# Optimization experiments

Measured on AMD Instinct MI355X. Metric: run time of the kernel, lower is better.

Reference implementation:

```python
import jax, jax.numpy as jnp
import numpy as np

B, T, C, HS = 8, 4096, 512, 64

def setup_inputs() -> dict:
    key = jax.random.key(0)
    k1, k2, k3, k4 = jax.random.split(key, 4)
    x = jax.random.normal(k1, (B, T, C), dtype=jnp.float32)
    # causal mask (lower-triangular), int32: 1 = keep, 0 = mask out
    mask = jnp.tril(jnp.ones((T, T), dtype=jnp.int32))
    Wk = jax.random.normal(k2, (C, HS), dtype=jnp.float32) * (1.0 / np.sqrt(C))
    Wq = jax.random.normal(k3, (C, HS), dtype=jnp.float32) * (1.0 / np.sqrt(C))
    Wv = jax.random.normal(k4, (C, HS), dtype=jnp.float32) * (1.0 / np.sqrt(C))
    return {"x": x, "mask": mask, "Wk": Wk, "Wq": Wq, "Wv": Wv}

def reference(x, mask, Wk, Wq, Wv):
    # single self-attention head; scale uses C (n_embd), matching the source
    k = jnp.einsum('btc,ch->bth', x, Wk)   # [B,T,HS]
    q = jnp.einsum('btc,ch->bth', x, Wq)
    v = jnp.einsum('btc,ch->bth', x, Wv)
    scale = x.shape[-1] ** -0.5
    wei = jnp.einsum('bth,bsh->bts', q, k) * scale          # [B,T,T]
    wei = jnp.where(mask == 0, jnp.float32(-1e9), wei)
    wei = jax.nn.softmax(wei, axis=-1)
    # dropout is identity in eval mode
    out = jnp.einsum('bts,bsh->bth', wei, v)                # [B,T,HS]
    return out
```

## Files before the change

kernel.cpp:

```cpp
#include <hip/hip_runtime.h>
#include <hip/hip_bf16.h>
#include <stdint.h>

typedef unsigned short u16;
typedef __bf16 bf16x8_t __attribute__((ext_vector_type(8)));
typedef __bf16 bf16x4_t __attribute__((ext_vector_type(4)));
typedef float f32x4_t __attribute__((ext_vector_type(4)));
typedef float f32x8_t __attribute__((ext_vector_type(8)));

#define TSEQ 4096
#define CDIM 512
#define HSD  64
#define NBATCH 8

static __device__ __forceinline__ f32x4_t mfma16(bf16x8_t a, bf16x8_t b, f32x4_t c) {
  return __builtin_amdgcn_mfma_f32_16x16x32_bf16(a, b, c, 0, 0, 0);
}

static __device__ __forceinline__ u16 f2bf(float f) {
  union { __bf16 h; u16 s; } v; v.h = (__bf16)f;
  return v.s;
}
static __device__ __forceinline__ float bf2f(u16 h) {
  union { unsigned u; float f; } v; v.u = ((unsigned)h) << 16;
  return v.f;
}
static __device__ __forceinline__ bf16x8_t pack8(const float* p) {
  f32x8_t v = *(const f32x8_t*)p;
  return __builtin_convertvector(v, bf16x8_t);
}
static __device__ __forceinline__ bf16x4_t cvt4(f32x4_t v) {
  return __builtin_convertvector(v, bf16x4_t);
}

static __device__ __forceinline__ void gload16(const void* g, void* l) {
  __builtin_amdgcn_global_load_lds(
      (const __attribute__((address_space(1))) unsigned int*)g,
      (__attribute__((address_space(3))) unsigned int*)l, 16, 0, 0);
}

#define QSCALE (0.044194173824159216f * 1.4426950408889634f)
#define MFIX 32.0f

__global__ __launch_bounds__(256) void repack_w(const float* __restrict__ Wk,
                                                const float* __restrict__ Wq,
                                                const float* __restrict__ Wv,
                                                u16* __restrict__ pw) {
  int i = blockIdx.x * 256 + threadIdx.x;
  int j    = i & 7;
  int l15  = (i >> 3) & 15;
  int quad = (i >> 7) & 3;
  int f    = i >> 9;
  int kc   = f / 12;
  int n12  = f - kc * 12;
  int m    = n12 >> 2;
  int n    = n12 & 3;
  const float* W = (m == 0) ? Wk : ((m == 1) ? Wq : Wv);
  pw[i] = f2bf(W[(kc * 32 + quad * 8 + j) * HSD + n * 16 + l15]);
}

__global__ __launch_bounds__(256, 2) void proj_kernel(const float* __restrict__ x,
                                                      const u16* __restrict__ pw,
                                                      u16* __restrict__ kb,
                                                      u16* __restrict__ qb,
                                                      u16* __restrict__ vb,
                                                      u16* __restrict__ vbT,
                                                      int split) {
  const int tid = threadIdx.x;
  const int lane = tid & 63;
  const int wave = tid >> 6;
  const int l15 = lane & 15, quad = lane >> 4;
  const int rblk = (int)blockIdx.x;
  const int rowLocal = wave * 16 + l15;

  __shared__ __align__(16) char SMEM[61440];
  float (*XS)[2048] = (float (*)[2048])SMEM;
  u16   (*PS)[6144] = (u16 (*)[6144])(SMEM + 24576);
  u16* VtS = (u16*)SMEM;

  const float* xg = x + (size_t)rblk * 64 * CDIM;

  const int xrow = tid >> 3;
  const int xch  = tid & 7;

  f32x4_t acc[12];
#pragma unroll
  for (int n = 0; n < 12; ++n) acc[n] = f32x4_t{0.f, 0.f, 0.f, 0.f};

  auto STAGE = [&](int slot, int kc) {
#pragma unroll
    for (int p = 0; p < 2; ++p) {
      const float* src = xg + (size_t)(p * 32 + xrow) * CDIM + kc * 32 + xch * 4;
      gload16(src, (char*)&XS[slot][0] + p * 4096 + tid * 16);
    }
#pragma unroll
    for (int r = 0; r < 3; ++r) {
      int f = r * 256 + tid;
      gload16(pw + (size_t)kc * 6144 + (size_t)f * 8, (char*)&PS[slot][0] + f * 16);
    }
  };

  STAGE(0, 0);
  STAGE(1, 1);

  int slot = 0;
  for (int kc = 0; kc < 16; ++kc) {
    if (kc < 15) asm volatile("s_waitcnt vmcnt(5)" ::: "memory");
    else         asm volatile("s_waitcnt vmcnt(0)" ::: "memory");
    __builtin_amdgcn_s_barrier();

    if (kc + 2 < 16) {
      int s2 = slot + 2; if (s2 >= 3) s2 -= 3;
      STAGE(s2, kc + 2);
    }

    f32x8_t xv = *(const f32x8_t*)&XS[slot][rowLocal * 32 + quad * 8];
    bf16x8_t a = __builtin_convertvector(xv, bf16x8_t);
#pragma unroll
    for (int n12 = 0; n12 < 12; ++n12) {
      bf16x8_t b = *(const bf16x8_t*)&PS[slot][((n12 * 4 + quad) * 16 + l15) * 8];
      acc[n12] = mfma16(a, b, acc[n12]);
    }

    ++slot; if (slot >= 3) slot = 0;
  }

  const int row_base = rblk * 64 + wave * 16 + quad * 4;
#pragma unroll
  for (int n = 0; n < 4; ++n) {
#pragma unroll
    for (int r = 0; r < 4; ++r) {
      kb[(size_t)(row_base + r) * HSD + n * 16 + l15] = f2bf(acc[n][r]);
      qb[(size_t)(row_base + r) * HSD + n * 16 + l15] = f2bf(acc[4 + n][r] * QSCALE);
    }
  }

  if (!split) {
#pragma unroll
    for (int n = 0; n < 4; ++n)
#pragma unroll
      for (int r = 0; r < 4; ++r)
        vb[(size_t)(row_base + r) * HSD + n * 16 + l15] = f2bf(acc[8 + n][r]);
  } else {
    __syncthreads();
#pragma unroll
    for (int n = 0; n < 4; ++n) {
      int h = n * 16 + l15;
      int tl = wave * 16 + quad * 4;
      *(bf16x4_t*)&VtS[h * 72 + tl] = cvt4(acc[8 + n]);
    }
    __syncthreads();
    const int bb = (rblk * 64) >> 12;
    const int t0 = (rblk * 64) & 4095;
#pragma unroll
    for (int it = 0; it < 2; ++it) {
      int g = it * 256 + tid;
      int h = g >> 3;
      int cc = g & 7;
      bf16x8_t vv = *(const bf16x8_t*)&VtS[h * 72 + cc * 8];
      *(bf16x8_t*)&vbT[(size_t)(bb * HSD + h) * TSEQ + t0 + cc * 8] = vv;
    }
  }
}

__global__ __launch_bounds__(256, 3) void attn_part(const u16* __restrict__ qb,
                                                    const u16* __restrict__ kb,
                                                    const u16* __restrict__ vbT,
                                                    u16* __restrict__ pO,
                                                    float* __restrict__ pl) {
  const int e = 287 - (int)blockIdx.x;
  int g = 0;
  while (g < 7 && 4 * (g + 1) * (g + 2) <= e) ++g;
  int local = e - 4 * g * (g + 1);
  int qtl = 0;
  while (local >= g + 1) { local -= g + 1; ++qtl; }
  const int qt = 8 * g + qtl;
  const int c  = local;

  const int b = blockIdx.y;
  const int tid = threadIdx.x;
  const int lane = tid & 63;
  const int wave = tid >> 6;
  const int l15 = lane & 15, quad = lane >> 4;

  __shared__ __align__(16) u16 Ks[128 * 72];
  __shared__ __align__(16) u16 Vt[64 * 136];
  __shared__ __align__(16) u16 Ps[4][16 * 72];

  const size_t bo = (size_t)b * TSEQ * HSD;
  const u16* qp = qb + bo;
  const u16* kp = kb + bo;
  const u16* vtp = vbT + (size_t)b * HSD * TSEQ;

  const int qglob = qt * 64 + wave * 16 + l15;
  bf16x8_t qf0 = *(const bf16x8_t*)(qp + (size_t)qglob * HSD + quad * 8);
  bf16x8_t qf1 = *(const bf16x8_t*)(qp + (size_t)qglob * HSD + 32 + quad * 8);

  f32x4_t o[4];
#pragma unroll
  for (int n = 0; n < 4; ++n) o[n] = f32x4_t{0.f, 0.f, 0.f, 0.f};
  float lsum = 0.f;

  const int st_lo = c * 8;
  const int nt = min(qt - st_lo + 1, 8);
  const int npair = (nt + 1) >> 1;

  const int kr = tid >> 3;
  const int kc8 = (tid & 7) * 8;
  const int vr = tid >> 4;
  const int vc8 = (tid & 15) * 8;

  u16* myP = Ps[wave];

  const f32x4_t sinit = f32x4_t{-MFIX, -MFIX, -MFIX, -MFIX};

  bf16x8_t kst[4], vst[4];
  {
    const int s64 = st_lo * 64;
#pragma unroll
    for (int p = 0; p < 4; ++p) {
      kst[p] = *(const bf16x8_t*)(kp + (size_t)(s64 + kr + 32 * p) * HSD + kc8);
      vst[p] = *(const bf16x8_t*)(vtp + (size_t)(vr + 16 * p) * TSEQ + s64 + vc8);
    }
  }

  for (int ip = 0; ip < npair; ++ip) {
    __syncthreads();
#pragma unroll
    for (int p = 0; p < 4; ++p) {
      *(bf16x8_t*)&Ks[(kr + 32 * p) * 72 + kc8] = kst[p];
      *(bf16x8_t*)&Vt[(vr + 16 * p) * 136 + vc8] = vst[p];
    }
    if (ip + 1 < npair) {
      const int s64 = (st_lo + 2 * (ip + 1)) * 64;
#pragma unroll
      for (int p = 0; p < 4; ++p) {
        kst[p] = *(const bf16x8_t*)(kp + (size_t)(s64 + kr + 32 * p) * HSD + kc8);
        vst[p] = *(const bf16x8_t*)(vtp + (size_t)(vr + 16 * p) * TSEQ + s64 + vc8);
      }
    }
    __syncthreads();

    const int st0 = st_lo + 2 * ip;
    const int nsub = (2 * ip + 1 < nt) ? 2 : 1;
#pragma unroll 2
    for (int hs = 0; hs < nsub; ++hs) {
      const int stx = st0 + hs;
      const int roff = hs * 64;

      f32x4_t s[4];
#pragma unroll
      for (int n = 0; n < 4; ++n) {
        bf16x8_t a0 = *(const bf16x8_t*)&Ks[(roff + n * 16 + l15) * 72 + quad * 8];
        bf16x8_t a1 = *(const bf16x8_t*)&Ks[(roff + n * 16 + l15) * 72 + 32 + quad * 8];
        f32x4_t a = sinit;
        a = mfma16(a0, qf0, a);
        a = mfma16(a1, qf1, a);
        s[n] = a;
      }

      if (stx == qt) {
#pragma unroll
        for (int n = 0; n < 4; ++n) {
          int sg = stx * 64 + n * 16 + quad * 4;
#pragma unroll
          for (int r = 0; r < 4; ++r)
            if (sg + r > qglob) s[n][r] = -1e9f;
        }
      }

#pragma unroll
      for (int n = 0; n < 4; ++n) {
        f32x4_t pv;
        pv[0] = exp2f(s[n][0]);
        pv[1] = exp2f(s[n][1]);
        pv[2] = exp2f(s[n][2]);
        pv[3] = exp2f(s[n][3]);
        lsum += (pv[0] + pv[1]) + (pv[2] + pv[3]);
        *(bf16x4_t*)&myP[l15 * 72 + n * 16 + quad * 4] = cvt4(pv);
      }

      asm volatile("s_waitcnt lgkmcnt(0)" ::: "memory");

#pragma unroll
      for (int kc = 0; kc < 2; ++kc) {
        bf16x8_t pf = *(const bf16x8_t*)&myP[l15 * 72 + kc * 32 + quad * 8];
#pragma unroll
        for (int n = 0; n < 4; ++n) {
          bf16x8_t vf = *(const bf16x8_t*)&Vt[(n * 16 + l15) * 136 + roff + kc * 32 + quad * 8];
          o[n] = mfma16(pf, vf, o[n]);
        }
      }
    }
  }

  lsum += __shfl_xor(lsum, 16);
  lsum += __shfl_xor(lsum, 32);

  const int pidx = (b * 64 + qt) * 8 + c;
  u16* po = pO + (size_t)pidx * 4096;
  float* pm = pl + (size_t)pidx * 64;
#pragma unroll
  for (int n = 0; n < 4; ++n)
#pragma unroll
    for (int r = 0; r < 4; ++r)
      po[(wave * 16 + quad * 4 + r) * 64 + n * 16 + l15] = f2bf(o[n][r]);
  if (lane < 16) pm[wave * 16 + lane] = lsum;
}

__global__ __launch_bounds__(256) void attn_combine(const u16* __restrict__ pO,
                                                    const float* __restrict__ pl,
                                                    float* __restrict__ out) {
  const int tid = threadIdx.x;
  const int h2 = tid & 31;
  const int rr = tid >> 5;
  const int rowg = blockIdx.x * 8 + rr;
  const int b = rowg >> 12;
  const int t = rowg & 4095;
  const int qt = t >> 6;
  const int tr = t & 63;
  const int nc = (qt >> 3) + 1;
  const int pbase = (b * 64 + qt) * 8;

  const unsigned* pO32 = (const unsigned*)pO;
  float o0 = 0.f, o1 = 0.f, lsum = 0.f;
  for (int cc = 0; cc < nc; ++cc) {
    lsum += pl[(size_t)(pbase + cc) * 64 + tr];
    unsigned u = pO32[(size_t)(pbase + cc) * 2048 + tr * 32 + h2];
    o0 += bf2f((u16)(u & 0xffffu));
    o1 += bf2f((u16)(u >> 16));
  }
  float2 res;
  res.x = o0 / lsum;
  res.y = o1 / lsum;
  *(float2*)&out[(size_t)rowg * HSD + h2 * 2] = res;
}

__global__ __launch_bounds__(256) void attn_single(const u16* __restrict__ qb,
                                                   const u16* __restrict__ kb,
                                                   const u16* __restrict__ vb,
                                                   float* __restrict__ out) {
  const int qt = (int)gridDim.x - 1 - (int)blockIdx.x;
  const int b = blockIdx.y;
  const int lane = threadIdx.x & 63;
  const int wave = threadIdx.x >> 6;
  const int l15 = lane & 15, quad = lane >> 4;

  __shared__ __align__(16) u16 Ks[64 * 72];
  __shared__ __align__(16) u16 Vt[64 * 72];
  __shared__ __align__(16) u16 Ps[4][16 * 72];

  const size_t bo = (size_t)b * TSEQ * HSD;
  const u16* qp = qb + bo;
  const u16* kp = kb + bo;
  const u16* vp = vb + bo;

  const int qrow0 = qt * 64 + wave * 16;
  bf16x8_t qf0 = *(const bf16x8_t*)(qp + (size_t)(qrow0 + l15) * HSD + quad * 8);
  bf16x8_t qf1 = *(const bf16x8_t*)(qp + (size_t)(qrow0 + l15) * HSD + 32 + quad * 8);

  f32x4_t o[4];
#pragma unroll
  for (int n = 0; n < 4; ++n) o[n] = f32x4_t{0.f, 0.f, 0.f, 0.f};
  float lrow[4] = {0.f, 0.f, 0.f, 0.f};

  const int ldr = threadIdx.x >> 3;
  const int ldc = (threadIdx.x & 7) * 8;

  const f32x4_t sinit = f32x4_t{-MFIX, -MFIX, -MFIX, -MFIX};

  for (int st = 0; st <= qt; ++st) {
    const int s0 = st * 64;
#pragma unroll
    for (int pp = 0; pp < 2; ++pp) {
      int r = ldr + pp * 32;
      bf16x8_t kv = *(const bf16x8_t*)(kp + (size_t)(s0 + r) * HSD + ldc);
      *(bf16x8_t*)&Ks[r * 72 + ldc] = kv;
      bf16x8_t vv = *(const bf16x8_t*)(vp + (size_t)(s0 + r) * HSD + ldc);
      const u16* vu = (const u16*)&vv;
#pragma unroll
      for (int j = 0; j < 8; ++j) Vt[(ldc + j) * 72 + r] = vu[j];
    }
    __syncthreads();

    f32x4_t s[4];
#pragma unroll
    for (int n = 0; n < 4; ++n) {
      bf16x8_t k0 = *(const bf16x8_t*)&Ks[(n * 16 + l15) * 72 + quad * 8];
      bf16x8_t k1 = *(const bf16x8_t*)&Ks[(n * 16 + l15) * 72 + 32 + quad * 8];
      f32x4_t a = sinit;
      a = mfma16(qf0, k0, a);
      a = mfma16(qf1, k1, a);
      s[n] = a;
    }

    if (st == qt) {
#pragma unroll
      for (int n = 0; n < 4; ++n) {
        int sg = s0 + n * 16 + l15;
#pragma unroll
        for (int r = 0; r < 4; ++r) {
          int tg = qrow0 + quad * 4 + r;
          if (sg > tg) s[n][r] = -1e9f;
        }
      }
    }

#pragma unroll
    for (int n = 0; n < 4; ++n)
#pragma unroll
      for (int r = 0; r < 4; ++r) {
        float p = exp2f(s[n][r]);
        s[n][r] = p;
        lrow[r] += p;
      }

    u16* myP = Ps[wave];
#pragma unroll
    for (int n = 0; n < 4; ++n)
#pragma unroll
      for (int r = 0; r < 4; ++r)
        myP[(quad * 4 + r) * 72 + n * 16 + l15] = f2bf(s[n][r]);

    __syncthreads();

#pragma unroll
    for (int kc = 0; kc < 2; ++kc) {
      bf16x8_t pf = *(const bf16x8_t*)&myP[l15 * 72 + kc * 32 + quad * 8];
#pragma unroll
      for (int n = 0; n < 4; ++n) {
        bf16x8_t vf = *(const bf16x8_t*)&Vt[(n * 16 + l15) * 72 + kc * 32 + quad * 8];
        o[n] = mfma16(pf, vf, o[n]);
      }
    }
    __syncthreads();
  }

#pragma unroll
  for (int r = 0; r < 4; ++r) {
    float l = lrow[r];
    l += __shfl_xor(l, 1);
    l += __shfl_xor(l, 2);
    l += __shfl_xor(l, 4);
    l += __shfl_xor(l, 8);
    lrow[r] = l;
  }

#pragma unroll
  for (int n = 0; n < 4; ++n)
#pragma unroll
    for (int r = 0; r < 4; ++r)
      out[bo + (size_t)(qrow0 + quad * 4 + r) * HSD + n * 16 + l15] = o[n][r] / lrow[r];
}

extern "C" void kernel_launch(void* const* d_in, const int* in_sizes, int n_in,
                              void* d_out, int out_size, void* d_ws, size_t ws_size,
                              hipStream_t stream) {
  const float* x  = (const float*)d_in[0];
  const float* Wk = (const float*)d_in[2];
  const float* Wq = (const float*)d_in[3];
  const float* Wv = (const float*)d_in[4];
  float* out = (float*)d_out;

  char* base = (char*)d_ws;
  const size_t KV = (size_t)NBATCH * TSEQ * HSD;
  u16* pw  = (u16*)base;
  u16* kb  = (u16*)(base + (1 << 18));
  u16* qb  = kb + KV;
  u16* vbT = qb + KV;
  u16* pO  = vbT + KV;
  u16* vb  = pO;
  float* pl = (float*)(pO + (size_t)4096 * 4096);
  const size_t need = (size_t)(1 << 18) + 3 * KV * 2
                    + (size_t)4096 * 4096 * 2
                    + (size_t)4096 * 64 * 4;
  const int split = (ws_size >= need) ? 1 : 0;

  hipLaunchKernelGGL(repack_w, dim3(384), dim3(256), 0, stream, Wk, Wq, Wv, pw);
  hipLaunchKernelGGL(proj_kernel, dim3(512), dim3(256), 0, stream, x, pw, kb, qb, vb, vbT, split);
  if (split) {
    hipLaunchKernelGGL(attn_part, dim3(288, NBATCH), dim3(256), 0, stream, qb, kb, vbT, pO, pl);
    hipLaunchKernelGGL(attn_combine, dim3(4096), dim3(256), 0, stream, pO, pl, out);
  } else {
    hipLaunchKernelGGL(attn_single, dim3(64, NBATCH), dim3(256), 0, stream, qb, kb, vb, out);
  }
}
```

Baseline: 195.9 us.

## Use 32x32 MFMA with 128-row query tiles and permlane P transfer

The attention-part kernel moves from 16x16x32 MFMA on 64-query tiles to 32x32x16 MFMA on 128-query tiles, so each block shares one K/V staging pass across twice as many queries and the grid is halved. The P matrix no longer round-trips through shared memory: it is rearranged in registers with permlane32_swap to form the A operand of the PV MFMA, which removes the Ps buffer and its LDS waits. Per-wave diagonal skipping drops key tiles that lie beyond a wave's causal limit. Occupancy is raised to 4 blocks per SM. The trade-offs are more accumulator registers and possibly coarser load balance across blocks.

```diff
diff --git a/kernel.cpp b/kernel.cpp
--- a/kernel.cpp
+++ b/kernel.cpp
@@ -7,6 +7,8 @@
 typedef __bf16 bf16x4_t __attribute__((ext_vector_type(4)));
 typedef float f32x4_t __attribute__((ext_vector_type(4)));
 typedef float f32x8_t __attribute__((ext_vector_type(8)));
+typedef float f32x16_t __attribute__((ext_vector_type(16)));
+typedef int i32x2_t __attribute__((ext_vector_type(2)));
 
 #define TSEQ 4096
 #define CDIM 512
@@ -15,6 +17,9 @@
 
 static __device__ __forceinline__ f32x4_t mfma16(bf16x8_t a, bf16x8_t b, f32x4_t c) {
   return __builtin_amdgcn_mfma_f32_16x16x32_bf16(a, b, c, 0, 0, 0);
+}
+static __device__ __forceinline__ f32x16_t mfma32(bf16x8_t a, bf16x8_t b, f32x16_t c) {
+  return __builtin_amdgcn_mfma_f32_32x32x16_bf16(a, b, c, 0, 0, 0);
 }
 
 static __device__ __forceinline__ u16 f2bf(float f) {
@@ -163,56 +168,56 @@
   }
 }
 
-__global__ __launch_bounds__(256, 3) void attn_part(const u16* __restrict__ qb,
+__global__ __launch_bounds__(256, 4) void attn_part(const u16* __restrict__ qb,
                                                     const u16* __restrict__ kb,
                                                     const u16* __restrict__ vbT,
                                                     u16* __restrict__ pO,
                                                     float* __restrict__ pl) {
-  const int e = 287 - (int)blockIdx.x;
+  const int e = 143 - (int)blockIdx.x;
   int g = 0;
-  while (g < 7 && 4 * (g + 1) * (g + 2) <= e) ++g;
-  int local = e - 4 * g * (g + 1);
+  while (g < 7 && 2 * (g + 1) * (g + 2) <= e) ++g;
+  int local = e - 2 * g * (g + 1);
   int qtl = 0;
   while (local >= g + 1) { local -= g + 1; ++qtl; }
-  const int qt = 8 * g + qtl;
-  const int c  = local;
+  const int qt2 = 4 * g + qtl;
+  const int c   = local;
 
   const int b = blockIdx.y;
   const int tid = threadIdx.x;
   const int lane = tid & 63;
   const int wave = tid >> 6;
-  const int l15 = lane & 15, quad = lane >> 4;
+  const int l31 = lane & 31;
+  const int h2  = lane >> 5;
 
   __shared__ __align__(16) u16 Ks[128 * 72];
   __shared__ __align__(16) u16 Vt[64 * 136];
-  __shared__ __align__(16) u16 Ps[4][16 * 72];
 
   const size_t bo = (size_t)b * TSEQ * HSD;
   const u16* qp = qb + bo;
   const u16* kp = kb + bo;
   const u16* vtp = vbT + (size_t)b * HSD * TSEQ;
 
-  const int qglob = qt * 64 + wave * 16 + l15;
-  bf16x8_t qf0 = *(const bf16x8_t*)(qp + (size_t)qglob * HSD + quad * 8);
-  bf16x8_t qf1 = *(const bf16x8_t*)(qp + (size_t)qglob * HSD + 32 + quad * 8);
-
-  f32x4_t o[4];
-#pragma unroll
-  for (int n = 0; n < 4; ++n) o[n] = f32x4_t{0.f, 0.f, 0.f, 0.f};
+  const int qglob = qt2 * 128 + wave * 32 + l31;
+  const int wdiag = (qt2 * 128 + wave * 32 + 31) >> 6;
+
+  bf16x8_t qf[4];
+#pragma unroll
+  for (int kk = 0; kk < 4; ++kk)
+    qf[kk] = *(const bf16x8_t*)(qp + (size_t)qglob * HSD + kk * 16 + h2 * 8);
+
+  f32x16_t o0, o1;
+#pragma unroll
+  for (int i = 0; i < 16; ++i) { o0[i] = 0.f; o1[i] = 0.f; }
   float lsum = 0.f;
 
   const int st_lo = c * 8;
-  const int nt = min(qt - st_lo + 1, 8);
+  const int nt = min(2 * qt2 + 2 - st_lo, 8);
   const int npair = (nt + 1) >> 1;
 
   const int kr = tid >> 3;
   const int kc8 = (tid & 7) * 8;
   const int vr = tid >> 4;
   const int vc8 = (tid & 15) * 8;
-
-  u16* myP = Ps[wave];
-
-  const f32x4_t sinit = f32x4_t{-MFIX, -MFIX, -MFIX, -MFIX};
 
   bf16x8_t kst[4], vst[4];
   {
@@ -246,66 +251,71 @@
 #pragma unroll 2
     for (int hs = 0; hs < nsub; ++hs) {
       const int stx = st0 + hs;
+      if (stx > wdiag) continue;
       const int roff = hs * 64;
 
-      f32x4_t s[4];
-#pragma unroll
-      for (int n = 0; n < 4; ++n) {
-        bf16x8_t a0 = *(const bf16x8_t*)&Ks[(roff + n * 16 + l15) * 72 + quad * 8];
-        bf16x8_t a1 = *(const bf16x8_t*)&Ks[(roff + n * 16 + l15) * 72 + 32 + quad * 8];
-        f32x4_t a = sinit;
-        a = mfma16(a0, qf0, a);
-        a = mfma16(a1, qf1, a);
-        s[n] = a;
-      }
-
-      if (stx == qt) {
-#pragma unroll
-        for (int n = 0; n < 4; ++n) {
-          int sg = stx * 64 + n * 16 + quad * 4;
-#pragma unroll
-          for (int r = 0; r < 4; ++r)
-            if (sg + r > qglob) s[n][r] = -1e9f;
+#pragma unroll
+      for (int st2 = 0; st2 < 2; ++st2) {
+        f32x16_t s;
+#pragma unroll
+        for (int i = 0; i < 16; ++i) s[i] = -MFIX;
+#pragma unroll
+        for (int kk = 0; kk < 4; ++kk) {
+          bf16x8_t a = *(const bf16x8_t*)&Ks[(roff + st2 * 32 + l31) * 72 + kk * 16 + h2 * 8];
+          s = mfma32(a, qf[kk], s);
+        }
+
+        if (stx == wdiag) {
+#pragma unroll
+          for (int i = 0; i < 16; ++i) {
+            int sg = stx * 64 + st2 * 32 + 4 * h2 + (i & 3) + 8 * (i >> 2);
+            if (sg > qglob) s[i] = -1e9f;
+          }
+        }
+
+#pragma unroll
+        for (int i = 0; i < 16; ++i) s[i] = exp2f(s[i]);
+#pragma unroll
+        for (int i = 0; i < 16; i += 4)
+          lsum += ((s[i] + s[i + 1]) + (s[i + 2] + s[i + 3]));
+
+        union { bf16x4_t v; int d[2]; } X[4];
+#pragma unroll
+        for (int m = 0; m < 4; ++m) {
+          f32x4_t t;
+          t[0] = s[4 * m]; t[1] = s[4 * m + 1]; t[2] = s[4 * m + 2]; t[3] = s[4 * m + 3];
+          X[m].v = cvt4(t);
+        }
+
+#pragma unroll
+        for (int kkl = 0; kkl < 2; ++kkl) {
+          i32x2_t r0 = __builtin_amdgcn_permlane32_swap(X[2 * kkl].d[0], X[2 * kkl + 1].d[0], false, false);
+          i32x2_t r1 = __builtin_amdgcn_permlane32_swap(X[2 * kkl].d[1], X[2 * kkl + 1].d[1], false, false);
+          union { bf16x8_t v; int d[4]; } af;
+          af.d[0] = r0[0]; af.d[1] = r1[0];
+          af.d[2] = r0[1]; af.d[3] = r1[1];
+          const int kkg = st2 * 2 + kkl;
+          bf16x8_t vf0 = *(const bf16x8_t*)&Vt[l31 * 136 + roff + kkg * 16 + h2 * 8];
+          bf16x8_t vf1 = *(const bf16x8_t*)&Vt[(32 + l31) * 136 + roff + kkg * 16 + h2 * 8];
+          o0 = mfma32(af.v, vf0, o0);
+          o1 = mfma32(af.v, vf1, o1);
         }
       }
-
-#pragma unroll
-      for (int n = 0; n < 4; ++n) {
-        f32x4_t pv;
-        pv[0] = exp2f(s[n][0]);
-        pv[1] = exp2f(s[n][1]);
-        pv[2] = exp2f(s[n][2]);
-        pv[3] = exp2f(s[n][3]);
-        lsum += (pv[0] + pv[1]) + (pv[2] + pv[3]);
-        *(bf16x4_t*)&myP[l15 * 72 + n * 16 + quad * 4] = cvt4(pv);
-      }
-
-      asm volatile("s_waitcnt lgkmcnt(0)" ::: "memory");
-
-#pragma unroll
-      for (int kc = 0; kc < 2; ++kc) {
-        bf16x8_t pf = *(const bf16x8_t*)&myP[l15 * 72 + kc * 32 + quad * 8];
-#pragma unroll
-        for (int n = 0; n < 4; ++n) {
-          bf16x8_t vf = *(const bf16x8_t*)&Vt[(n * 16 + l15) * 136 + roff + kc * 32 + quad * 8];
-          o[n] = mfma16(pf, vf, o[n]);
-        }
-      }
-    }
-  }
-
-  lsum += __shfl_xor(lsum, 16);
+    }
+  }
+
   lsum += __shfl_xor(lsum, 32);
 
-  const int pidx = (b * 64 + qt) * 8 + c;
+  const int pidx = (b * 64 + 2 * qt2 + (wave >> 1)) * 8 + c;
   u16* po = pO + (size_t)pidx * 4096;
   float* pm = pl + (size_t)pidx * 64;
 #pragma unroll
-  for (int n = 0; n < 4; ++n)
-#pragma unroll
-    for (int r = 0; r < 4; ++r)
-      po[(wave * 16 + quad * 4 + r) * 64 + n * 16 + l15] = f2bf(o[n][r]);
-  if (lane < 16) pm[wave * 16 + lane] = lsum;
+  for (int i = 0; i < 16; ++i) {
+    int rloc = (wave & 1) * 32 + 4 * h2 + (i & 3) + 8 * (i >> 2);
+    po[rloc * 64 + l31]      = f2bf(o0[i]);
+    po[rloc * 64 + 32 + l31] = f2bf(o1[i]);
+  }
+  if (lane < 32) pm[(wave & 1) * 32 + lane] = lsum;
 }
 
 __global__ __launch_bounds__(256) void attn_combine(const u16* __restrict__ pO,
@@ -479,7 +489,7 @@
   hipLaunchKernelGGL(repack_w, dim3(384), dim3(256), 0, stream, Wk, Wq, Wv, pw);
   hipLaunchKernelGGL(proj_kernel, dim3(512), dim3(256), 0, stream, x, pw, kb, qb, vb, vbT, split);
   if (split) {
-    hipLaunchKernelGGL(attn_part, dim3(288, NBATCH), dim3(256), 0, stream, qb, kb, vbT, pO, pl);
+    hipLaunchKernelGGL(attn_part, dim3(144, NBATCH), dim3(256), 0, stream, qb, kb, vbT, pO, pl);
     hipLaunchKernelGGL(attn_combine, dim3(4096), dim3(256), 0, stream, pO, pl, out);
   } else {
     hipLaunchKernelGGL(attn_single, dim3(64, NBATCH), dim3(256), 0, stream, qb, kb, vb, out);
```

Measured after the change: 215.1 us. 1.1x slower.
